# Kernel tuning notes

Measured on AMD Instinct MI355X. Metric: run time of the kernel, lower is better.

Reference implementation:

```python
import jax, jax.numpy as jnp
import numpy as np

B, T, V, H, OUT = 1024, 128, 89, 256, 1


def setup_inputs() -> dict:
    key = jax.random.key(0)
    ks = jax.random.split(key, 16)
    x = jax.random.normal(ks[0], (B, T, V), dtype=jnp.float32)
    mask = (jax.random.uniform(ks[1], (B, T, V)) < 0.7).astype(jnp.float32)
    deltas = jax.random.uniform(ks[2], (B, T, V), dtype=jnp.float32)
    meanset = jax.random.normal(ks[3], (V,), dtype=jnp.float32)

    def uni(k, shape, fan):
        s = 1.0 / np.sqrt(fan)
        return jax.random.uniform(k, shape, jnp.float32, -s, s)

    # Decay h: Linear(V -> H); Decay x: diag Linear(V -> V)
    W_h = uni(ks[4], (H, V), V)
    b_h = uni(ks[5], (H,), V)
    W_x = uni(ks[6], (V, V), V)
    b_x = uni(ks[7], (V,), V)
    # GRUCell(2V -> H), torch layout: W_ih [3H, 2V], W_hh [3H, H]
    W_ih = uni(ks[8], (3 * H, 2 * V), 2 * V)
    b_ih = uni(ks[9], (3 * H,), 2 * V)
    W_hh = uni(ks[10], (3 * H, H), H)
    b_hh = uni(ks[11], (3 * H,), H)
    # classification head
    W_cls = uni(ks[12], (OUT, H), H)
    b_cls = uni(ks[13], (OUT,), H)
    return {"x": x, "mask": mask, "deltas": deltas, "meanset": meanset,
            "W_h": W_h, "b_h": b_h, "W_x": W_x, "b_x": b_x,
            "W_ih": W_ih, "b_ih": b_ih, "W_hh": W_hh, "b_hh": b_hh,
            "W_cls": W_cls, "b_cls": b_cls}


def reference(x, mask, deltas, meanset, W_h, b_h, W_x, b_x,
              W_ih, b_ih, W_hh, b_hh, W_cls, b_cls):
    Bn, Tn, Vn = x.shape
    Hn = W_h.shape[0]
    # diag Decay: W * eye(V) -> only the diagonal of W_x contributes
    w_x_diag = jnp.diagonal(W_x)

    def step(carry, inp):
        h, last, loss = carry
        x_t, m_t, d_t = inp  # each [B, V]
        gamma_h = jnp.exp(-jax.nn.relu(d_t @ W_h.T + b_h))          # [B, H]
        gamma_x = jnp.exp(-jax.nn.relu(d_t * w_x_diag + b_x))       # [B, V]
        # forward-fill (pandas ffill includes current observation)
        last = jnp.where(m_t > 0, x_t, last)
        h = h * gamma_h
        x_u = gamma_x * last + (1.0 - gamma_x) * meanset
        loss = loss + jnp.sum(jnp.abs(x_t - x_u) * m_t) / (jnp.sum(m_t) + 1e-5)
        x_h = m_t * x_t + (1.0 - m_t) * x_u
        inp_cat = jnp.concatenate([x_h, m_t], axis=1)               # [B, 2V]
        gi = inp_cat @ W_ih.T + b_ih
        gh = h @ W_hh.T + b_hh
        i_r, i_z, i_n = jnp.split(gi, 3, axis=1)
        h_r, h_z, h_n = jnp.split(gh, 3, axis=1)
        r = jax.nn.sigmoid(i_r + h_r)
        z = jax.nn.sigmoid(i_z + h_z)
        n = jnp.tanh(i_n + r * h_n)
        h = (1.0 - z) * n + z * h
        return (h, last, loss), x_h

    init = (jnp.zeros((Bn, Hn), x.dtype), jnp.zeros((Bn, Vn), x.dtype),
            jnp.zeros((), x.dtype))
    xs = (jnp.swapaxes(x, 0, 1), jnp.swapaxes(mask, 0, 1), jnp.swapaxes(deltas, 0, 1))
    (h, _, x_loss), ximp = jax.lax.scan(step, init, xs)
    x_imp = jnp.swapaxes(ximp, 0, 1)                                # [B, T, V]
    # dropout is identity at eval time
    y_out = h @ W_cls.T + b_cls
    y_score = jax.nn.sigmoid(y_out)
    return x_imp, x_loss, y_out, y_score
```

## Files before the change

kernel.cpp:

```cpp
#include <hip/hip_runtime.h>

#define B_  1024
#define T_  128
#define V_  89
#define H_  256
#define NB2 256
#define PT_ 4
#define NPH 32

typedef __attribute__((ext_vector_type(8))) short bf16x8;
typedef __attribute__((ext_vector_type(4))) float f32x4;
typedef __attribute__((ext_vector_type(4))) unsigned short u16x4;

__device__ __forceinline__ short f2bs(float f){
    unsigned u = __float_as_uint(f);
    unsigned r = (u + 0x7FFFu + ((u>>16)&1u)) >> 16;
    return (short)r;
}
__device__ __forceinline__ float s2f(unsigned short s){
    return __uint_as_float(((unsigned)s) << 16);
}
__device__ __forceinline__ float sig_(float x){ return 1.f/(1.f+__expf(-x)); }
__device__ __forceinline__ float tanh_(float x){ return 2.f/(1.f+__expf(-2.f*x)) - 1.f; }

__global__ __launch_bounds__(256) void k_cvt_fp8(
    const float* __restrict__ src, unsigned char* __restrict__ dst, int n)
{
    int i = blockIdx.x*256 + threadIdx.x;
    if (i*4 >= n) return;
    float f0 = src[i*4+0], f1 = src[i*4+1], f2 = src[i*4+2], f3 = src[i*4+3];
    int w = __builtin_amdgcn_cvt_pk_fp8_f32(f0, f1, 0, false);
    w     = __builtin_amdgcn_cvt_pk_fp8_f32(f2, f3, w, true);
    ((int*)dst)[i] = w;
}

__global__ __launch_bounds__(256) void k_prep_wih8(
    const float* __restrict__ W_ih, const float* __restrict__ b_ih,
    unsigned char* __restrict__ dst)
{
    int i = blockIdx.x*256 + threadIdx.x;
    if (i >= 768*48) return;
    int n = i / 48, k4 = (i - n*48)*4;
    float f[4];
    #pragma unroll
    for (int j = 0; j < 4; ++j) {
        int k = k4 + j;
        f[j] = (k < 178) ? W_ih[(size_t)n*178 + k] : (k == 178 ? b_ih[n] : 0.f);
    }
    int w = __builtin_amdgcn_cvt_pk_fp8_f32(f[0], f[1], 0, false);
    w     = __builtin_amdgcn_cvt_pk_fp8_f32(f[2], f[3], w, true);
    ((int*)dst)[i] = w;
}

__global__ __launch_bounds__(256) void k_prep_whp(
    const float* __restrict__ W_h, const float* __restrict__ b_h,
    short* __restrict__ dst)
{
    int i = blockIdx.x*256 + threadIdx.x;
    if (i >= 256*96) return;
    int n = i / 96, k = i - n*96;
    float v = (k < V_) ? W_h[(size_t)n*V_ + k] : (k == V_ ? b_h[n] : 0.f);
    dst[i] = f2bs(v);
}

__global__ __launch_bounds__(256) void k_gammah(
    const float* __restrict__ deltas, const short* __restrict__ whp,
    unsigned short* __restrict__ gdv)
{
    __shared__ short dl2[16*104] __attribute__((aligned(16)));
    int tid = threadIdx.x;
    int bx = blockIdx.x, p = blockIdx.y;
    for (int i = tid; i < 16*96; i += 256) {
        int m = i / 96, k = i - m*96;
        int b = bx*4 + (m>>2), t = p*4 + (m&3);
        float val = 0.f;
        if (k < V_)       val = deltas[((size_t)b*T_ + t)*V_ + k];
        else if (k == V_) val = 1.0f;
        dl2[m*104 + k] = f2bs(val);
    }
    __syncthreads();
    int lane = tid & 63, wv = tid >> 6;
    int l15 = lane & 15, g8 = lane >> 4;
    f32x4 z4 = {0.f,0.f,0.f,0.f};
    f32x4 acc[4];
    #pragma unroll
    for (int nt = 0; nt < 4; ++nt) acc[nt] = z4;
    #pragma unroll
    for (int kt = 0; kt < 3; ++kt) {
        bf16x8 a = *(const bf16x8*)&dl2[l15*104 + kt*32 + g8*8];
        #pragma unroll
        for (int nt = 0; nt < 4; ++nt) {
            int cg = wv*64 + nt*16 + l15;
            bf16x8 bb = *(const bf16x8*)(whp + (size_t)cg*96 + kt*32 + g8*8);
            acc[nt] = __builtin_amdgcn_mfma_f32_16x16x32_bf16(a, bb, acc[nt], 0,0,0);
        }
    }
    #pragma unroll
    for (int nt = 0; nt < 4; ++nt) {
        int cg = wv*64 + nt*16 + l15;
        u16x4 v;
        #pragma unroll
        for (int rr = 0; rr < 4; ++rr)
            v[rr] = (unsigned short)f2bs(__expf(-fmaxf(acc[nt][rr], 0.f)));
        ((u16x4*)gdv)[((size_t)(p*1024 + bx*4 + g8))*256 + cg] = v;
    }
}

__global__ __launch_bounds__(512)
__attribute__((amdgpu_waves_per_eu(2, 2)))
void k_fused(
    const float* __restrict__ x, const float* __restrict__ mask,
    const float* __restrict__ deltas, const float* __restrict__ meanset,
    const float* __restrict__ W_x, const float* __restrict__ b_x,
    const unsigned char* __restrict__ wihb8, const unsigned char* __restrict__ whh8,
    const unsigned short* __restrict__ gdv, const float* __restrict__ b_hh,
    const float* __restrict__ W_cls, const float* __restrict__ b_cls,
    float* __restrict__ ximp, float* __restrict__ numpart, float* __restrict__ denpart,
    float* __restrict__ yout, float* __restrict__ yscore)
{
    __shared__ unsigned char xl[16*200] __attribute__((aligned(16)));
    __shared__ unsigned char hlds[2][4*272] __attribute__((aligned(16)));
    __shared__ float lossn[PT_][360], lossd[PT_][360];
    __shared__ float yred[4][8];

    int tid = threadIdx.x;
    int lane = tid & 63, wv = tid >> 6;
    int l15 = lane & 15, g8 = lane >> 4;
    int blk = blockIdx.x;
    int c0 = wv*16 + l15;
    int c1 = c0 + 128;

    for (int i = tid; i < 16*14; i += 512) {
        int r = i / 14, k = 178 + (i - r*14);
        xl[r*200 + k] = (k == 178) ? 0x38 : 0;
    }

    bool own = (tid < 4*V_);
    int r_o = tid / V_, v_o = tid - r_o*V_;
    int b_o = blk*4 + r_o;
    float wxd = 0.f, bx = 0.f, mnv = 0.f, last = 0.f;
    if (own) { wxd = W_x[v_o*V_ + v_o]; bx = b_x[v_o]; mnv = meanset[v_o]; }

    long wih0[3][6], wih1[3][6], wf0[3][8], wf1[3][8];
    #pragma unroll
    for (int g = 0; g < 3; ++g) {
        #pragma unroll
        for (int kt = 0; kt < 6; ++kt) {
            wih0[g][kt] = *(const long*)(wihb8 + (size_t)(g*H_ + c0)*192 + kt*32 + g8*8);
            wih1[g][kt] = *(const long*)(wihb8 + (size_t)(g*H_ + c1)*192 + kt*32 + g8*8);
        }
        #pragma unroll
        for (int kt = 0; kt < 8; ++kt) {
            wf0[g][kt] = *(const long*)(whh8 + (size_t)(g*H_ + c0)*H_ + kt*32 + g8*8);
            wf1[g][kt] = *(const long*)(whh8 + (size_t)(g*H_ + c1)*H_ + kt*32 + g8*8);
        }
    }
    #pragma unroll
    for (int g = 0; g < 3; ++g) {
        #pragma unroll
        for (int kt = 0; kt < 6; ++kt) {
            asm volatile("" : "+v"(wih0[g][kt]));
            asm volatile("" : "+v"(wih1[g][kt]));
        }
        #pragma unroll
        for (int kt = 0; kt < 8; ++kt) {
            asm volatile("" : "+v"(wf0[g][kt]));
            asm volatile("" : "+v"(wf1[g][kt]));
        }
    }
    float bhh00 = b_hh[c0], bhh10 = b_hh[H_ + c0], bhh20 = b_hh[2*H_ + c0];
    float bhh01 = b_hh[c1], bhh11 = b_hh[H_ + c1], bhh21 = b_hh[2*H_ + c1];

    float h0 = 0.f, h1 = 0.f;

    for (int p = 0; p < NPH; ++p) {
        u16x4 gdl0 = ((const u16x4*)gdv)[((size_t)(p*1024 + blk*4 + g8))*256 + c0];
        u16x4 gdl1 = ((const u16x4*)gdv)[((size_t)(p*1024 + blk*4 + g8))*256 + c1];

        if (own) {
            const float* xb = x      + ((size_t)b_o*T_ + p*PT_)*V_ + v_o;
            const float* mb = mask   + ((size_t)b_o*T_ + p*PT_)*V_ + v_o;
            const float* db = deltas + ((size_t)b_o*T_ + p*PT_)*V_ + v_o;
            float xv[PT_], mv[PT_], dv[PT_];
            #pragma unroll
            for (int lt = 0; lt < PT_; ++lt) {
                xv[lt] = xb[lt*V_]; mv[lt] = mb[lt*V_]; dv[lt] = db[lt*V_];
            }
            #pragma unroll
            for (int lt = 0; lt < PT_; ++lt) {
                float xt = xv[lt], m = mv[lt], d = dv[lt];
                float gx = __expf(-fmaxf(fmaf(d, wxd, bx), 0.f));
                last = (m > 0.f) ? xt : last;
                float xu = gx*last + (1.f-gx)*mnv;
                float xh = m*xt + (1.f-m)*xu;
                ximp[((size_t)b_o*T_ + p*PT_ + lt)*V_ + v_o] = xh;
                int mr = r_o*4 + lt;
                int pk = __builtin_amdgcn_cvt_pk_fp8_f32(xh, m, 0, false);
                xl[mr*200 + v_o]      = (unsigned char)(pk & 0xFF);
                xl[mr*200 + V_ + v_o] = (unsigned char)((pk >> 8) & 0xFF);
                lossn[lt][tid] = fabsf(xt - xu)*m;
                lossd[lt][tid] = m;
            }
        }
        __syncthreads();

        if (tid < 64) {
            int lt = tid >> 4, part = tid & 15;
            float n = 0.f, ds = 0.f;
            for (int j = part; j < 4*V_; j += 16) { n += lossn[lt][j]; ds += lossd[lt][j]; }
            n += __shfl_xor(n, 1); ds += __shfl_xor(ds, 1);
            n += __shfl_xor(n, 2); ds += __shfl_xor(ds, 2);
            n += __shfl_xor(n, 4); ds += __shfl_xor(ds, 4);
            n += __shfl_xor(n, 8); ds += __shfl_xor(ds, 8);
            if (part == 0) {
                int t = p*PT_ + lt;
                numpart[t*NB2 + blk] = n;
                denpart[t*NB2 + blk] = ds;
            }
        }

        f32x4 ar0 = {0.f,0.f,0.f,0.f}, az0 = ar0, an0 = ar0;
        f32x4 ar1 = ar0, az1 = ar0, an1 = ar0;
        #pragma unroll
        for (int kt = 0; kt < 6; ++kt) {
            long a = *(const long*)&xl[l15*200 + kt*32 + g8*8];
            ar0 = __builtin_amdgcn_mfma_f32_16x16x32_fp8_fp8(a, wih0[0][kt], ar0, 0,0,0);
            az0 = __builtin_amdgcn_mfma_f32_16x16x32_fp8_fp8(a, wih0[1][kt], az0, 0,0,0);
            an0 = __builtin_amdgcn_mfma_f32_16x16x32_fp8_fp8(a, wih0[2][kt], an0, 0,0,0);
            ar1 = __builtin_amdgcn_mfma_f32_16x16x32_fp8_fp8(a, wih1[0][kt], ar1, 0,0,0);
            az1 = __builtin_amdgcn_mfma_f32_16x16x32_fp8_fp8(a, wih1[1][kt], az1, 0,0,0);
            an1 = __builtin_amdgcn_mfma_f32_16x16x32_fp8_fp8(a, wih1[2][kt], an1, 0,0,0);
        }

        #pragma unroll
        for (int lt = 0; lt < PT_; ++lt) {
            const int cb = lt & 1;
            float hd0 = h0 * s2f(gdl0[lt]);
            float hd1 = h1 * s2f(gdl1[lt]);
            int pk = __builtin_amdgcn_cvt_pk_fp8_f32(hd0, hd1, 0, false);
            hlds[cb][g8*272 + c0] = (unsigned char)(pk & 0xFF);
            hlds[cb][g8*272 + c1] = (unsigned char)((pk >> 8) & 0xFF);
            __syncthreads();
            f32x4 s00 = {bhh00,bhh00,bhh00,bhh00};
            f32x4 s10 = {bhh10,bhh10,bhh10,bhh10};
            f32x4 s20 = {bhh20,bhh20,bhh20,bhh20};
            f32x4 s01 = {bhh01,bhh01,bhh01,bhh01};
            f32x4 s11 = {bhh11,bhh11,bhh11,bhh11};
            f32x4 s21 = {bhh21,bhh21,bhh21,bhh21};
            #pragma unroll
            for (int kt = 0; kt < 8; ++kt) {
                long a = *(const long*)&hlds[cb][(l15>>2)*272 + kt*32 + g8*8];
                s00 = __builtin_amdgcn_mfma_f32_16x16x32_fp8_fp8(a, wf0[0][kt], s00, 0,0,0);
                s10 = __builtin_amdgcn_mfma_f32_16x16x32_fp8_fp8(a, wf0[1][kt], s10, 0,0,0);
                s20 = __builtin_amdgcn_mfma_f32_16x16x32_fp8_fp8(a, wf0[2][kt], s20, 0,0,0);
                s01 = __builtin_amdgcn_mfma_f32_16x16x32_fp8_fp8(a, wf1[0][kt], s01, 0,0,0);
                s11 = __builtin_amdgcn_mfma_f32_16x16x32_fp8_fp8(a, wf1[1][kt], s11, 0,0,0);
                s21 = __builtin_amdgcn_mfma_f32_16x16x32_fp8_fp8(a, wf1[2][kt], s21, 0,0,0);
            }
            float rg0 = sig_(ar0[lt] + s00[0]);
            float zg0 = sig_(az0[lt] + s10[0]);
            float ng0 = tanh_(an0[lt] + rg0*s20[0]);
            h0 = (1.f - zg0)*ng0 + zg0*hd0;
            float rg1 = sig_(ar1[lt] + s01[0]);
            float zg1 = sig_(az1[lt] + s11[0]);
            float ng1 = tanh_(an1[lt] + rg1*s21[0]);
            h1 = (1.f - zg1)*ng1 + zg1*hd1;
        }
    }

    {
        float pr = h0 * W_cls[c0] + h1 * W_cls[c1];
        pr += __shfl_xor(pr, 1);
        pr += __shfl_xor(pr, 2);
        pr += __shfl_xor(pr, 4);
        pr += __shfl_xor(pr, 8);
        if (l15 == 0) yred[g8][wv] = pr;
        __syncthreads();
        if (tid < 4) {
            float s = b_cls[0];
            #pragma unroll
            for (int ww = 0; ww < 8; ++ww) s += yred[tid][ww];
            yout[blk*4 + tid]   = s;
            yscore[blk*4 + tid] = 1.f/(1.f+__expf(-s));
        }
    }
}

__global__ __launch_bounds__(256) void k_loss_t(
    const float* __restrict__ numpart, const float* __restrict__ denpart,
    float* __restrict__ tpart)
{
    int t = blockIdx.x, tid = threadIdx.x;
    float n = numpart[t*NB2 + tid];
    float d = denpart[t*NB2 + tid];
    for (int off = 32; off; off >>= 1) { n += __shfl_down(n, off); d += __shfl_down(d, off); }
    __shared__ float sn[4], sd[4];
    int lane = tid & 63, wid = tid >> 6;
    if (lane == 0) { sn[wid] = n; sd[wid] = d; }
    __syncthreads();
    if (tid == 0) {
        float nn = sn[0]+sn[1]+sn[2]+sn[3], dd = sd[0]+sd[1]+sd[2]+sd[3];
        tpart[t] = nn / (dd + 1e-5f);
    }
}

__global__ __launch_bounds__(128) void k_loss_final(
    const float* __restrict__ tpart, float* __restrict__ out_loss)
{
    int tid = threadIdx.x;
    float s = tpart[tid];
    for (int off = 32; off; off >>= 1) s += __shfl_down(s, off);
    __shared__ float sp[2];
    if ((tid&63)==0) sp[tid>>6] = s;
    __syncthreads();
    if (tid==0) out_loss[0] = sp[0] + sp[1];
}

static inline size_t al256(size_t x){ return (x + 255) & ~(size_t)255; }

extern "C" void kernel_launch(void* const* d_in, const int* in_sizes, int n_in,
                              void* d_out, int out_size, void* d_ws, size_t ws_size,
                              hipStream_t stream)
{
    const float* x      = (const float*)d_in[0];
    const float* mask   = (const float*)d_in[1];
    const float* deltas = (const float*)d_in[2];
    const float* meanset= (const float*)d_in[3];
    const float* W_h    = (const float*)d_in[4];
    const float* b_h    = (const float*)d_in[5];
    const float* W_x    = (const float*)d_in[6];
    const float* b_x    = (const float*)d_in[7];
    const float* W_ih   = (const float*)d_in[8];
    const float* b_ih   = (const float*)d_in[9];
    const float* W_hh   = (const float*)d_in[10];
    const float* b_hh   = (const float*)d_in[11];
    const float* W_cls  = (const float*)d_in[12];
    const float* b_cls  = (const float*)d_in[13];

    float* out    = (float*)d_out;
    float* ximp   = out;
    float* xloss  = out + (size_t)B_*T_*V_;
    float* yout   = xloss + 1;
    float* yscore = yout + B_;

    size_t off = 0;
    size_t off_whh8 = off; off = al256(off + (size_t)768*256);
    size_t off_wih8 = off; off = al256(off + (size_t)768*192);
    size_t off_whp  = off; off = al256(off + (size_t)256*96*2);
    size_t off_gdv  = off; off = al256(off + (size_t)B_*T_*H_*2);
    size_t off_np   = off; off = al256(off + (size_t)T_*NB2*4);
    size_t off_dp   = off; off = al256(off + (size_t)T_*NB2*4);
    size_t off_tp   = off; off = al256(off + (size_t)T_*4);
    if (off > ws_size) return;

    char* ws = (char*)d_ws;
    unsigned char* whh8 = (unsigned char*)(ws + off_whh8);
    unsigned char* wih8 = (unsigned char*)(ws + off_wih8);
    short* whp    = (short*)(ws + off_whp);
    unsigned short* gdv = (unsigned short*)(ws + off_gdv);
    float* numpart= (float*)(ws + off_np);
    float* denpart= (float*)(ws + off_dp);
    float* tpart  = (float*)(ws + off_tp);

    hipLaunchKernelGGL(k_cvt_fp8, dim3((768*256/4+255)/256), dim3(256), 0, stream, W_hh, whh8, 768*256);
    hipLaunchKernelGGL(k_prep_wih8, dim3((768*48+255)/256), dim3(256), 0, stream, W_ih, b_ih, wih8);
    hipLaunchKernelGGL(k_prep_whp, dim3((256*96+255)/256), dim3(256), 0, stream, W_h, b_h, whp);
    hipLaunchKernelGGL(k_gammah, dim3(256, 32), dim3(256), 0, stream, deltas, whp, gdv);
    hipLaunchKernelGGL(k_fused, dim3(NB2), dim3(512), 0, stream,
                       x, mask, deltas, meanset, W_x, b_x,
                       wih8, whh8, gdv, b_hh, W_cls, b_cls,
                       ximp, numpart, denpart, yout, yscore);
    hipLaunchKernelGGL(k_loss_t, dim3(T_), dim3(256), 0, stream, numpart, denpart, tpart);
    hipLaunchKernelGGL(k_loss_final, dim3(1), dim3(128), 0, stream, tpart, xloss);
}
```

Measured before the change: 315.3 us.

## Move GRU weights out of registers into LDS and L2, prefetch next-phase inputs

The W_hh r/z gate weights now sit in a 128KB XOR-swizzled shared-memory tile, and only the n-gate weights stay in registers. The W_ih weights are repacked into an MFMA-fragment-ordered layout and read from global memory (L2) on every phase. The x/mask/deltas and gamma_h loads for the next phase are issued early to overlap the MFMA work. This lowers register pressure and may avoid spills or allow scheduling freedom, at the cost of extra LDS and global read traffic inside the serial recurrence loop.

```diff
diff --git a/kernel.cpp b/kernel.cpp
--- a/kernel.cpp
+++ b/kernel.cpp
@@ -39,17 +39,24 @@
     unsigned char* __restrict__ dst)
 {
     int i = blockIdx.x*256 + threadIdx.x;
-    if (i >= 768*48) return;
-    int n = i / 48, k4 = (i - n*48)*4;
-    float f[4];
-    #pragma unroll
-    for (int j = 0; j < 4; ++j) {
-        int k = k4 + j;
+    if (i >= 18432) return;
+    int l15 = i & 15, t = i >> 4;
+    int g8 = t & 3; t >>= 2;
+    int kt = t % 6; t /= 6;
+    int g = t % 3, WV = t / 3;
+    int n = g*256 + WV*16 + l15;
+    float f[8];
+    #pragma unroll
+    for (int j = 0; j < 8; ++j) {
+        int k = kt*32 + g8*8 + j;
         f[j] = (k < 178) ? W_ih[(size_t)n*178 + k] : (k == 178 ? b_ih[n] : 0.f);
     }
-    int w = __builtin_amdgcn_cvt_pk_fp8_f32(f[0], f[1], 0, false);
-    w     = __builtin_amdgcn_cvt_pk_fp8_f32(f[2], f[3], w, true);
-    ((int*)dst)[i] = w;
+    int w0 = __builtin_amdgcn_cvt_pk_fp8_f32(f[0], f[1], 0, false);
+    w0     = __builtin_amdgcn_cvt_pk_fp8_f32(f[2], f[3], w0, true);
+    int w1 = __builtin_amdgcn_cvt_pk_fp8_f32(f[4], f[5], 0, false);
+    w1     = __builtin_amdgcn_cvt_pk_fp8_f32(f[6], f[7], w1, true);
+    ((int*)dst)[i*2]   = w0;
+    ((int*)dst)[i*2+1] = w1;
 }
 
 __global__ __launch_bounds__(256) void k_prep_whp(
@@ -106,18 +113,18 @@
     }
 }
 
-__global__ __launch_bounds__(512)
-__attribute__((amdgpu_waves_per_eu(2, 2)))
+__global__ __launch_bounds__(512, 2)
 void k_fused(
     const float* __restrict__ x, const float* __restrict__ mask,
     const float* __restrict__ deltas, const float* __restrict__ meanset,
     const float* __restrict__ W_x, const float* __restrict__ b_x,
-    const unsigned char* __restrict__ wihb8, const unsigned char* __restrict__ whh8,
+    const unsigned char* __restrict__ wihT, const unsigned char* __restrict__ whh8,
     const unsigned short* __restrict__ gdv, const float* __restrict__ b_hh,
     const float* __restrict__ W_cls, const float* __restrict__ b_cls,
     float* __restrict__ ximp, float* __restrict__ numpart, float* __restrict__ denpart,
     float* __restrict__ yout, float* __restrict__ yscore)
 {
+    __shared__ unsigned char whL[512*256];
     __shared__ unsigned char xl[16*200] __attribute__((aligned(16)));
     __shared__ unsigned char hlds[2][4*272] __attribute__((aligned(16)));
     __shared__ float lossn[PT_][360], lossd[PT_][360];
@@ -129,11 +136,32 @@
     int blk = blockIdx.x;
     int c0 = wv*16 + l15;
     int c1 = c0 + 128;
-
+    int mR = (c0 & 31) << 3;
+
+    for (int idx = tid; idx < 512*32; idx += 512) {
+        int row = idx >> 5, j = idx & 31;
+        long v = *(const long*)(whh8 + (size_t)row*256 + j*8);
+        *(long*)&whL[row*256 + ((j*8) ^ ((row & 31) << 3))] = v;
+    }
     for (int i = tid; i < 16*14; i += 512) {
         int r = i / 14, k = 178 + (i - r*14);
         xl[r*200 + k] = (k == 178) ? 0x38 : 0;
     }
+
+    long wfn0[8], wfn1[8];
+    #pragma unroll
+    for (int kt = 0; kt < 8; ++kt) {
+        wfn0[kt] = *(const long*)(whh8 + (size_t)(512 + c0)*256 + kt*32 + g8*8);
+        wfn1[kt] = *(const long*)(whh8 + (size_t)(512 + c1)*256 + kt*32 + g8*8);
+    }
+    #pragma unroll
+    for (int kt = 0; kt < 8; ++kt) {
+        asm volatile("" : "+v"(wfn0[kt]));
+        asm volatile("" : "+v"(wfn1[kt]));
+    }
+
+    float bhr0 = b_hh[c0], bhz0 = b_hh[H_ + c0], bhn0 = b_hh[2*H_ + c0];
+    float bhr1 = b_hh[c1], bhz1 = b_hh[H_ + c1], bhn1 = b_hh[2*H_ + c1];
 
     bool own = (tid < 4*V_);
     int r_o = tid / V_, v_o = tid - r_o*V_;
@@ -141,54 +169,30 @@
     float wxd = 0.f, bx = 0.f, mnv = 0.f, last = 0.f;
     if (own) { wxd = W_x[v_o*V_ + v_o]; bx = b_x[v_o]; mnv = meanset[v_o]; }
 
-    long wih0[3][6], wih1[3][6], wf0[3][8], wf1[3][8];
-    #pragma unroll
-    for (int g = 0; g < 3; ++g) {
+    const long* wT = (const long*)wihT;
+    int iw0 = wv*1152 + g8*16 + l15;
+    int iw1 = (wv + 8)*1152 + g8*16 + l15;
+
+    float h0 = 0.f, h1 = 0.f;
+
+    float xv[PT_], mv[PT_], dvv[PT_];
+    if (own) {
+        const float* xb = x      + ((size_t)b_o*T_)*V_ + v_o;
+        const float* mb = mask   + ((size_t)b_o*T_)*V_ + v_o;
+        const float* db = deltas + ((size_t)b_o*T_)*V_ + v_o;
         #pragma unroll
-        for (int kt = 0; kt < 6; ++kt) {
-            wih0[g][kt] = *(const long*)(wihb8 + (size_t)(g*H_ + c0)*192 + kt*32 + g8*8);
-            wih1[g][kt] = *(const long*)(wihb8 + (size_t)(g*H_ + c1)*192 + kt*32 + g8*8);
-        }
-        #pragma unroll
-        for (int kt = 0; kt < 8; ++kt) {
-            wf0[g][kt] = *(const long*)(whh8 + (size_t)(g*H_ + c0)*H_ + kt*32 + g8*8);
-            wf1[g][kt] = *(const long*)(whh8 + (size_t)(g*H_ + c1)*H_ + kt*32 + g8*8);
-        }
-    }
-    #pragma unroll
-    for (int g = 0; g < 3; ++g) {
-        #pragma unroll
-        for (int kt = 0; kt < 6; ++kt) {
-            asm volatile("" : "+v"(wih0[g][kt]));
-            asm volatile("" : "+v"(wih1[g][kt]));
-        }
-        #pragma unroll
-        for (int kt = 0; kt < 8; ++kt) {
-            asm volatile("" : "+v"(wf0[g][kt]));
-            asm volatile("" : "+v"(wf1[g][kt]));
-        }
-    }
-    float bhh00 = b_hh[c0], bhh10 = b_hh[H_ + c0], bhh20 = b_hh[2*H_ + c0];
-    float bhh01 = b_hh[c1], bhh11 = b_hh[H_ + c1], bhh21 = b_hh[2*H_ + c1];
-
-    float h0 = 0.f, h1 = 0.f;
+        for (int lt = 0; lt < PT_; ++lt) {
+            xv[lt] = xb[lt*V_]; mv[lt] = mb[lt*V_]; dvv[lt] = db[lt*V_];
+        }
+    }
+    u16x4 gdl0 = ((const u16x4*)gdv)[((size_t)(blk*4 + g8))*256 + c0];
+    u16x4 gdl1 = ((const u16x4*)gdv)[((size_t)(blk*4 + g8))*256 + c1];
 
     for (int p = 0; p < NPH; ++p) {
-        u16x4 gdl0 = ((const u16x4*)gdv)[((size_t)(p*1024 + blk*4 + g8))*256 + c0];
-        u16x4 gdl1 = ((const u16x4*)gdv)[((size_t)(p*1024 + blk*4 + g8))*256 + c1];
-
         if (own) {
-            const float* xb = x      + ((size_t)b_o*T_ + p*PT_)*V_ + v_o;
-            const float* mb = mask   + ((size_t)b_o*T_ + p*PT_)*V_ + v_o;
-            const float* db = deltas + ((size_t)b_o*T_ + p*PT_)*V_ + v_o;
-            float xv[PT_], mv[PT_], dv[PT_];
             #pragma unroll
             for (int lt = 0; lt < PT_; ++lt) {
-                xv[lt] = xb[lt*V_]; mv[lt] = mb[lt*V_]; dv[lt] = db[lt*V_];
-            }
-            #pragma unroll
-            for (int lt = 0; lt < PT_; ++lt) {
-                float xt = xv[lt], m = mv[lt], d = dv[lt];
+                float xt = xv[lt], m = mv[lt], d = dvv[lt];
                 float gx = __expf(-fmaxf(fmaf(d, wxd, bx), 0.f));
                 last = (m > 0.f) ? xt : last;
                 float xu = gx*last + (1.f-gx)*mnv;
@@ -224,14 +228,35 @@
         #pragma unroll
         for (int kt = 0; kt < 6; ++kt) {
             long a = *(const long*)&xl[l15*200 + kt*32 + g8*8];
-            ar0 = __builtin_amdgcn_mfma_f32_16x16x32_fp8_fp8(a, wih0[0][kt], ar0, 0,0,0);
-            az0 = __builtin_amdgcn_mfma_f32_16x16x32_fp8_fp8(a, wih0[1][kt], az0, 0,0,0);
-            an0 = __builtin_amdgcn_mfma_f32_16x16x32_fp8_fp8(a, wih0[2][kt], an0, 0,0,0);
-            ar1 = __builtin_amdgcn_mfma_f32_16x16x32_fp8_fp8(a, wih1[0][kt], ar1, 0,0,0);
-            az1 = __builtin_amdgcn_mfma_f32_16x16x32_fp8_fp8(a, wih1[1][kt], az1, 0,0,0);
-            an1 = __builtin_amdgcn_mfma_f32_16x16x32_fp8_fp8(a, wih1[2][kt], an1, 0,0,0);
-        }
-
+            ar0 = __builtin_amdgcn_mfma_f32_16x16x32_fp8_fp8(a, wT[iw0 +         kt*64], ar0, 0,0,0);
+            az0 = __builtin_amdgcn_mfma_f32_16x16x32_fp8_fp8(a, wT[iw0 + 384 +   kt*64], az0, 0,0,0);
+            an0 = __builtin_amdgcn_mfma_f32_16x16x32_fp8_fp8(a, wT[iw0 + 768 +   kt*64], an0, 0,0,0);
+            ar1 = __builtin_amdgcn_mfma_f32_16x16x32_fp8_fp8(a, wT[iw1 +         kt*64], ar1, 0,0,0);
+            az1 = __builtin_amdgcn_mfma_f32_16x16x32_fp8_fp8(a, wT[iw1 + 384 +   kt*64], az1, 0,0,0);
+            an1 = __builtin_amdgcn_mfma_f32_16x16x32_fp8_fp8(a, wT[iw1 + 768 +   kt*64], an1, 0,0,0);
+        }
+
+        if (p + 1 < NPH) {
+            if (own) {
+                const float* xb = x      + ((size_t)b_o*T_ + (p+1)*PT_)*V_ + v_o;
+                const float* mb = mask   + ((size_t)b_o*T_ + (p+1)*PT_)*V_ + v_o;
+                const float* db = deltas + ((size_t)b_o*T_ + (p+1)*PT_)*V_ + v_o;
+                #pragma unroll
+                for (int lt = 0; lt < PT_; ++lt) {
+                    xv[lt] = xb[lt*V_]; mv[lt] = mb[lt*V_]; dvv[lt] = db[lt*V_];
+                }
+            }
+        }
+        u16x4 ngdl0 = gdl0, ngdl1 = gdl1;
+        if (p + 1 < NPH) {
+            ngdl0 = ((const u16x4*)gdv)[((size_t)((p+1)*1024 + blk*4 + g8))*256 + c0];
+            ngdl1 = ((const u16x4*)gdv)[((size_t)((p+1)*1024 + blk*4 + g8))*256 + c1];
+        }
+
+        const unsigned char* wr0 = whL + (size_t)c0*256;
+        const unsigned char* wr1 = whL + (size_t)(c0+128)*256;
+        const unsigned char* wz0 = whL + (size_t)(c0+256)*256;
+        const unsigned char* wz1 = whL + (size_t)(c0+384)*256;
         #pragma unroll
         for (int lt = 0; lt < PT_; ++lt) {
             const int cb = lt & 1;
@@ -241,21 +266,22 @@
             hlds[cb][g8*272 + c0] = (unsigned char)(pk & 0xFF);
             hlds[cb][g8*272 + c1] = (unsigned char)((pk >> 8) & 0xFF);
             __syncthreads();
-            f32x4 s00 = {bhh00,bhh00,bhh00,bhh00};
-            f32x4 s10 = {bhh10,bhh10,bhh10,bhh10};
-            f32x4 s20 = {bhh20,bhh20,bhh20,bhh20};
-            f32x4 s01 = {bhh01,bhh01,bhh01,bhh01};
-            f32x4 s11 = {bhh11,bhh11,bhh11,bhh11};
-            f32x4 s21 = {bhh21,bhh21,bhh21,bhh21};
+            f32x4 s00 = {bhr0,bhr0,bhr0,bhr0};
+            f32x4 s10 = {bhz0,bhz0,bhz0,bhz0};
+            f32x4 s20 = {bhn0,bhn0,bhn0,bhn0};
+            f32x4 s01 = {bhr1,bhr1,bhr1,bhr1};
+            f32x4 s11 = {bhz1,bhz1,bhz1,bhz1};
+            f32x4 s21 = {bhn1,bhn1,bhn1,bhn1};
             #pragma unroll
             for (int kt = 0; kt < 8; ++kt) {
                 long a = *(const long*)&hlds[cb][(l15>>2)*272 + kt*32 + g8*8];
-                s00 = __builtin_amdgcn_mfma_f32_16x16x32_fp8_fp8(a, wf0[0][kt], s00, 0,0,0);
-                s10 = __builtin_amdgcn_mfma_f32_16x16x32_fp8_fp8(a, wf0[1][kt], s10, 0,0,0);
-                s20 = __builtin_amdgcn_mfma_f32_16x16x32_fp8_fp8(a, wf0[2][kt], s20, 0,0,0);
-                s01 = __builtin_amdgcn_mfma_f32_16x16x32_fp8_fp8(a, wf1[0][kt], s01, 0,0,0);
-                s11 = __builtin_amdgcn_mfma_f32_16x16x32_fp8_fp8(a, wf1[1][kt], s11, 0,0,0);
-                s21 = __builtin_amdgcn_mfma_f32_16x16x32_fp8_fp8(a, wf1[2][kt], s21, 0,0,0);
+                int o = (kt*32 + g8*8) ^ mR;
+                s00 = __builtin_amdgcn_mfma_f32_16x16x32_fp8_fp8(a, *(const long*)(wr0 + o), s00, 0,0,0);
+                s01 = __builtin_amdgcn_mfma_f32_16x16x32_fp8_fp8(a, *(const long*)(wr1 + o), s01, 0,0,0);
+                s10 = __builtin_amdgcn_mfma_f32_16x16x32_fp8_fp8(a, *(const long*)(wz0 + o), s10, 0,0,0);
+                s11 = __builtin_amdgcn_mfma_f32_16x16x32_fp8_fp8(a, *(const long*)(wz1 + o), s11, 0,0,0);
+                s20 = __builtin_amdgcn_mfma_f32_16x16x32_fp8_fp8(a, wfn0[kt], s20, 0,0,0);
+                s21 = __builtin_amdgcn_mfma_f32_16x16x32_fp8_fp8(a, wfn1[kt], s21, 0,0,0);
             }
             float rg0 = sig_(ar0[lt] + s00[0]);
             float zg0 = sig_(az0[lt] + s10[0]);
@@ -266,6 +292,7 @@
             float ng1 = tanh_(an1[lt] + rg1*s21[0]);
             h1 = (1.f - zg1)*ng1 + zg1*hd1;
         }
+        gdl0 = ngdl0; gdl1 = ngdl1;
     }
 
     {
@@ -363,7 +390,7 @@
     float* tpart  = (float*)(ws + off_tp);
 
     hipLaunchKernelGGL(k_cvt_fp8, dim3((768*256/4+255)/256), dim3(256), 0, stream, W_hh, whh8, 768*256);
-    hipLaunchKernelGGL(k_prep_wih8, dim3((768*48+255)/256), dim3(256), 0, stream, W_ih, b_ih, wih8);
+    hipLaunchKernelGGL(k_prep_wih8, dim3((18432+255)/256), dim3(256), 0, stream, W_ih, b_ih, wih8);
     hipLaunchKernelGGL(k_prep_whp, dim3((256*96+255)/256), dim3(256), 0, stream, W_h, b_h, whp);
     hipLaunchKernelGGL(k_gammah, dim3(256, 32), dim3(256), 0, stream, deltas, whp, gdv);
     hipLaunchKernelGGL(k_fused, dim3(NB2), dim3(512), 0, stream,
```

Measured after the change: 370.6 us. 1.18x slower.
